# Kernel optimization log

Hardware: AMD Instinct MI355X
Metric: run time of the kernel (lower is better)

Reference implementation:

```python
import jax, jax.numpy as jnp
import numpy as np

IN_FEATURES = 4096
OUT_FEATURES = 11008
TOKENS = 4096


def setup_inputs() -> dict:
    key = jax.random.key(0)
    k1, k2, k3, k4 = jax.random.split(key, 4)
    x = jax.random.normal(k1, (TOKENS, IN_FEATURES), dtype=jnp.float32)
    # two int4 nibbles per byte; aligned_in == IN_FEATURES (already multiple of 64)
    weight_packed = jax.random.randint(k2, (OUT_FEATURES, IN_FEATURES // 2), 0, 256, dtype=jnp.int32).astype(jnp.uint8)
    scale = jax.random.uniform(k3, (OUT_FEATURES, 1), dtype=jnp.float32, minval=0.005, maxval=0.02)
    zero = jax.random.uniform(k4, (OUT_FEATURES, 1), dtype=jnp.float32, minval=0.0, maxval=15.0)
    return {"x": x, "weight_packed": weight_packed, "scale": scale, "zero": zero}


def reference(x, weight_packed, scale, zero):
    # unpack nibbles, low_first order (default OMNICODER_INT4_NIBBLE_ORDER)
    low = (weight_packed & jnp.uint8(0x0F)).astype(jnp.float32)
    high = ((weight_packed >> 4) & jnp.uint8(0x0F)).astype(jnp.float32)
    # (O, K/2, 2) -> (O, K): interleave [low, high] per byte
    nibbles = jnp.stack((low, high), axis=-1).reshape(weight_packed.shape[0], -1)
    # dequantize with per-output-channel scale/zero
    w = (nibbles - zero) * scale          # (O, aligned_in)
    w = w[:, :IN_FEATURES]                # trim alignment padding (no-op here)
    return x @ w.T                        # (TOKENS, O)
```

## Files before the change

### kernel.cpp

```cpp
#include <hip/hip_runtime.h>
#include <hip/hip_fp16.h>
#include <stdint.h>

#define TOKENS 4096
#define IN_F   4096
#define OUT_F  11008

typedef _Float16 half8 __attribute__((ext_vector_type(8)));
typedef float    f32x4 __attribute__((ext_vector_type(4)));

union H4 { __half2 h2[2]; uint2 u2; };
union H8 { __half2 h2[4]; uint4 u4; };

#define GLOAD16(g, l) __builtin_amdgcn_global_load_lds(                      \
    (const __attribute__((address_space(1))) uint32_t*)(g),                  \
    (__attribute__((address_space(3))) uint32_t*)(l), 16, 0, 0)

__global__ __launch_bounds__(256)
void convert_x_kernel(const float* __restrict__ x, __half* __restrict__ x16)
{
  const size_t i = ((size_t)blockIdx.x * 256 + threadIdx.x) * 8;
  const float4 a = *reinterpret_cast<const float4*>(x + i);
  const float4 b = *reinterpret_cast<const float4*>(x + i + 4);
  H8 r;
  r.h2[0] = __floats2half2_rn(a.x, a.y);
  r.h2[1] = __floats2half2_rn(a.z, a.w);
  r.h2[2] = __floats2half2_rn(b.x, b.y);
  r.h2[3] = __floats2half2_rn(b.z, b.w);
  *reinterpret_cast<uint4*>(x16 + i) = r.u4;
}

__global__ __launch_bounds__(256)
void dequant_w_kernel(const int* __restrict__ wq,
                      const float* __restrict__ scale,
                      const float* __restrict__ zero,
                      __half* __restrict__ w16)
{
  const size_t i = ((size_t)blockIdx.x * 256 + threadIdx.x) * 4;
  const int row = (int)(i >> 11);
  const float s  = scale[row];
  const float nb = -zero[row] * s;
  const int4 v = *reinterpret_cast<const int4*>(wq + i);
  H8 r;
  r.h2[0] = __floats2half2_rn(fmaf((float)(v.x & 15), s, nb),
                              fmaf((float)((v.x >> 4) & 15), s, nb));
  r.h2[1] = __floats2half2_rn(fmaf((float)(v.y & 15), s, nb),
                              fmaf((float)((v.y >> 4) & 15), s, nb));
  r.h2[2] = __floats2half2_rn(fmaf((float)(v.z & 15), s, nb),
                              fmaf((float)((v.z >> 4) & 15), s, nb));
  r.h2[3] = __floats2half2_rn(fmaf((float)(v.w & 15), s, nb),
                              fmaf((float)((v.w >> 4) & 15), s, nb));
  *reinterpret_cast<uint4*>(w16 + i * 2) = r.u4;
}


#define VMW4 asm volatile("s_waitcnt vmcnt(4)" ::: "memory")

#define STAGE_A(H, K0, LB)                                                    \
  do {                                                                        \
    GLOAD16(apst + (H) * 128 * IN_F + (K0), &smem[(LB) + c0 * 512]);          \
    GLOAD16(apst + (H) * 128 * IN_F + 8 * IN_F + (K0),                        \
            &smem[(LB) + c0 * 512 + 512]);                                    \
  } while (0)

#define STAGE_B(H, K0, LB)                                                    \
  do {                                                                        \
    GLOAD16(bpst + (H) * 128 * IN_F + (K0), &smem[(LB) + c0 * 512]);          \
    GLOAD16(bpst + (H) * 128 * IN_F + 8 * IN_F + (K0),                        \
            &smem[(LB) + c0 * 512 + 512]);                                    \
  } while (0)

#define PHASE(BUF, MB, READB, STAGE_STMT, DOWAIT)                             \
  do {                                                                        \
    const int _ar = arootA + (BUF) * 32768;                                   \
    const int _br = brootB + (BUF) * 32768;                                   \
    if (READB) {                                                              \
      _Pragma("unroll")                                                       \
      for (int _j = 0; _j < 4; ++_j) {                                        \
        const int _rh = bn_rh + _j * 16;                                      \
        bfr[_j][0] = *(const half8*)&smem[_br + _rh * 64 + acol0];            \
        bfr[_j][1] = *(const half8*)&smem[_br + _rh * 64 + acol1];            \
      }                                                                       \
    }                                                                         \
    half8 _af[2][2];                                                          \
    _Pragma("unroll")                                                         \
    for (int _ii = 0; _ii < 2; ++_ii) {                                       \
      const int _rh = am_rh + ((MB) * 2 + _ii) * 16;                          \
      _af[_ii][0] = *(const half8*)&smem[_ar + _rh * 64 + acol0];             \
      _af[_ii][1] = *(const half8*)&smem[_ar + _rh * 64 + acol1];             \
    }                                                                         \
    STAGE_STMT;                                                               \
    __builtin_amdgcn_sched_barrier(0);                                        \
    __builtin_amdgcn_s_barrier();                                             \
    asm volatile("s_waitcnt lgkmcnt(0)" ::: "memory");                        \
    __builtin_amdgcn_sched_barrier(0);                                        \
    __builtin_amdgcn_s_setprio(1);                                            \
    _Pragma("unroll")                                                         \
    for (int _ii = 0; _ii < 2; ++_ii)                                         \
      _Pragma("unroll")                                                       \
      for (int _j = 0; _j < 4; ++_j) {                                        \
        acc[(MB) * 2 + _ii][_j] = __builtin_amdgcn_mfma_f32_16x16x32_f16(     \
            _af[_ii][0], bfr[_j][0], acc[(MB) * 2 + _ii][_j], 0, 0, 0);       \
        acc[(MB) * 2 + _ii][_j] = __builtin_amdgcn_mfma_f32_16x16x32_f16(     \
            _af[_ii][1], bfr[_j][1], acc[(MB) * 2 + _ii][_j], 0, 0, 0);       \
      }                                                                       \
    __builtin_amdgcn_s_setprio(0);                                            \
    if (DOWAIT) { VMW4; }                                                     \
    __builtin_amdgcn_sched_barrier(0);                                        \
    __builtin_amdgcn_s_barrier();                                             \
  } while (0)

__global__ __launch_bounds__(512, 2)
void gemm256_kernel(const __half* __restrict__ A16,
                    const __half* __restrict__ W16,
                    float* __restrict__ out)
{
  __shared__ __half smem[65536];

  const int bid = blockIdx.x;
  const int wg  = (bid & 7) * 86 + (bid >> 3);
  const int mt  = wg / 43;
  const int nt  = wg - mt * 43;
  const int m0  = mt * 256;
  const int n0  = nt * 256;

  const int tid  = threadIdx.x;
  const int lane = tid & 63;
  const int wave = tid >> 6;
  const int wr   = wave >> 2;
  const int wc   = wave & 3;
  const int fm   = lane & 15;
  const int q4   = lane >> 4;

  const int swz   = (fm & 7) << 3;
  const int acol0 = (q4 * 8) ^ swz;
  const int acol1 = (32 + q4 * 8) ^ swz;
  const int arootA = wr * 8192;
  const int brootB = 16384 + (wc >> 1) * 8192;
  const int am_rh  = fm;
  const int bn_rh  = (wc & 1) * 64 + fm;

  const int c0 = wave * 2;
  const int sr = lane >> 3;
  const int sc = ((lane & 7) ^ sr) * 8;
  const __half* apst = A16 + (size_t)(m0 + c0 * 8 + sr) * IN_F + sc;
  const __half* bpst = W16 + (size_t)(n0 + c0 * 8 + sr) * IN_F + sc;

  f32x4 acc[8][4];
#pragma unroll
  for (int i = 0; i < 8; ++i)
#pragma unroll
    for (int j = 0; j < 4; ++j)
      acc[i][j] = (f32x4){0.f, 0.f, 0.f, 0.f};

  half8 bfr[4][2];

  STAGE_B(0, 0, 16384);
  STAGE_B(1, 0, 16384 + 8192);
  STAGE_A(0, 0, 0);
  STAGE_A(1, 0, 8192);
  STAGE_B(0, 64, 32768 + 16384);
  STAGE_B(1, 64, 32768 + 16384 + 8192);
  VMW4;
  __builtin_amdgcn_sched_barrier(0);
  __builtin_amdgcn_s_barrier();

#pragma unroll 1
  for (int it = 0; it < 32; ++it) {
    const int k_o = (it * 2 + 1) * 64;
    const int ke2 = ((it * 2 + 2) & 63) * 64;
    const int ko2 = ((it * 2 + 3) & 63) * 64;
    PHASE(0, 0, 1, STAGE_A(0, k_o, 32768 + 0),            0);
    PHASE(0, 1, 0, STAGE_A(1, k_o, 32768 + 8192),         0);
    PHASE(0, 2, 0, STAGE_B(0, ke2, 16384),                0);
    PHASE(0, 3, 0, STAGE_B(1, ke2, 16384 + 8192),         1);
    PHASE(1, 0, 1, STAGE_A(0, ke2, 0),                    0);
    PHASE(1, 1, 0, STAGE_A(1, ke2, 8192),                 0);
    PHASE(1, 2, 0, STAGE_B(0, ko2, 32768 + 16384),        0);
    PHASE(1, 3, 0, STAGE_B(1, ko2, 32768 + 16384 + 8192), 1);
  }

  asm volatile("s_waitcnt vmcnt(0)" ::: "memory");

  const int mbase = m0 + wr * 128 + q4 * 4;
  const int nbase = n0 + wc * 64 + fm;
#pragma unroll
  for (int i = 0; i < 8; ++i) {
#pragma unroll
    for (int j = 0; j < 4; ++j) {
#pragma unroll
      for (int r = 0; r < 4; ++r) {
        out[(size_t)(mbase + i * 16 + r) * OUT_F + (nbase + j * 16)] = acc[i][j][r];
      }
    }
  }
}

#define BM  128
#define BN  128
#define BK  32
#define LDT 40
#define NKT (IN_F / BK)

__device__ inline __half2 dequant_byte(int v, __half2 s2, __half2 b2) {
  float lo = (float)(v & 15);
  float hi = (float)((v >> 4) & 15);
  return __hfma2(__floats2half2_rn(lo, hi), s2, b2);
}

__global__ __launch_bounds__(256, 2)
void int4_gemm_kernel(const float* __restrict__ x,
                      const int* __restrict__ wq,
                      const float* __restrict__ scale,
                      const float* __restrict__ zero,
                      float* __restrict__ out)
{
  __shared__ __half As[BM * LDT];
  __shared__ __half Bs[BN * LDT];

  const int tid  = threadIdx.x;
  const int n0   = blockIdx.x * BN;
  const int m0   = blockIdx.y * BM;
  const int lane = tid & 63;
  const int wave = tid >> 6;
  const int wm   = (wave >> 1) * 64;
  const int wn   = (wave & 1) * 64;

  const int rowb  = tid >> 1;
  const int bhalf = tid & 1;
  const float s = scale[n0 + rowb];
  const float z = zero[n0 + rowb];
  const __half2 s2 = __floats2half2_rn(s, s);
  const float   nb = -z * s;
  const __half2 b2 = __floats2half2_rn(nb, nb);
  const int* wp = wq + (size_t)(n0 + rowb) * (IN_F / 2) + bhalf * 8;

  const float* xp[4];
  int arow[4], ac4[4];
#pragma unroll
  for (int i = 0; i < 4; ++i) {
    int idx = tid + i * 256;
    arow[i] = idx >> 3;
    ac4[i]  = idx & 7;
    xp[i] = x + (size_t)(m0 + arow[i]) * IN_F + ac4[i] * 4;
  }

  f32x4 acc[4][4];
#pragma unroll
  for (int i = 0; i < 4; ++i)
#pragma unroll
    for (int j = 0; j < 4; ++j)
      acc[i][j] = (f32x4){0.f, 0.f, 0.f, 0.f};

  float4 apf[4];
  int4   bpf0, bpf1;
#pragma unroll
  for (int i = 0; i < 4; ++i) apf[i] = *(const float4*)(xp[i]);
  bpf0 = *(const int4*)(wp);
  bpf1 = *(const int4*)(wp + 4);

  for (int kt = 0; kt < NKT; ++kt) {
#pragma unroll
    for (int i = 0; i < 4; ++i) {
      H4 t;
      t.h2[0] = __floats2half2_rn(apf[i].x, apf[i].y);
      t.h2[1] = __floats2half2_rn(apf[i].z, apf[i].w);
      *reinterpret_cast<uint2*>(&As[arow[i] * LDT + ac4[i] * 4]) = t.u2;
    }
    {
      H8 r0, r1;
      r0.h2[0] = dequant_byte(bpf0.x, s2, b2);
      r0.h2[1] = dequant_byte(bpf0.y, s2, b2);
      r0.h2[2] = dequant_byte(bpf0.z, s2, b2);
      r0.h2[3] = dequant_byte(bpf0.w, s2, b2);
      r1.h2[0] = dequant_byte(bpf1.x, s2, b2);
      r1.h2[1] = dequant_byte(bpf1.y, s2, b2);
      r1.h2[2] = dequant_byte(bpf1.z, s2, b2);
      r1.h2[3] = dequant_byte(bpf1.w, s2, b2);
      *reinterpret_cast<uint4*>(&Bs[rowb * LDT + bhalf * 16 + 0]) = r0.u4;
      *reinterpret_cast<uint4*>(&Bs[rowb * LDT + bhalf * 16 + 8]) = r1.u4;
    }
    if (kt + 1 < NKT) {
#pragma unroll
      for (int i = 0; i < 4; ++i) apf[i] = *(const float4*)(xp[i] + (kt + 1) * BK);
      bpf0 = *(const int4*)(wp + (size_t)(kt + 1) * 16);
      bpf1 = *(const int4*)(wp + (size_t)(kt + 1) * 16 + 4);
    }
    __syncthreads();

    const int fm = lane & 15;
    const int q4 = lane >> 4;
    half8 af[4], bf[4];
#pragma unroll
    for (int i = 0; i < 4; ++i)
      af[i] = *reinterpret_cast<const half8*>(&As[(wm + i * 16 + fm) * LDT + q4 * 8]);
#pragma unroll
    for (int j = 0; j < 4; ++j)
      bf[j] = *reinterpret_cast<const half8*>(&Bs[(wn + j * 16 + fm) * LDT + q4 * 8]);
#pragma unroll
    for (int i = 0; i < 4; ++i)
#pragma unroll
      for (int j = 0; j < 4; ++j)
        acc[i][j] = __builtin_amdgcn_mfma_f32_16x16x32_f16(af[i], bf[j], acc[i][j], 0, 0, 0);
    __syncthreads();
  }

  const int col = lane & 15;
  const int r0q = (lane >> 4) * 4;
#pragma unroll
  for (int i = 0; i < 4; ++i) {
#pragma unroll
    for (int j = 0; j < 4; ++j) {
#pragma unroll
      for (int r = 0; r < 4; ++r) {
        const int m = m0 + wm + i * 16 + r0q + r;
        const int n = n0 + wn + j * 16 + col;
        out[(size_t)m * OUT_F + n] = acc[i][j][r];
      }
    }
  }
}

extern "C" void kernel_launch(void* const* d_in, const int* in_sizes, int n_in,
                              void* d_out, int out_size, void* d_ws, size_t ws_size,
                              hipStream_t stream) {
  const float* x     = (const float*)d_in[0];
  const int*   wq    = (const int*)d_in[1];
  const float* scale = (const float*)d_in[2];
  const float* zero  = (const float*)d_in[3];
  float* out = (float*)d_out;

  const size_t X16_BYTES = (size_t)TOKENS * IN_F * sizeof(__half);
  const size_t W16_BYTES = (size_t)OUT_F * IN_F * sizeof(__half);

  if (ws_size >= X16_BYTES + W16_BYTES) {
    __half* x16 = (__half*)d_ws;
    __half* w16 = (__half*)((char*)d_ws + X16_BYTES);
    convert_x_kernel<<<(TOKENS * IN_F / 8) / 256, 256, 0, stream>>>(x, x16);
    dequant_w_kernel<<<(OUT_F * (IN_F / 2) / 4) / 256, 256, 0, stream>>>(wq, scale, zero, w16);
    gemm256_kernel<<<dim3((OUT_F / 256) * (TOKENS / 256)), 512, 0, stream>>>(x16, w16, out);
  } else {
    dim3 grid(OUT_F / BN, TOKENS / BM);
    int4_gemm_kernel<<<grid, 256, 0, stream>>>(x, wq, scale, zero, out);
  }
}
```

Baseline: 619.4 us.

## Interleave A rows across waves for per-phase waits and merge prepass kernels

The GEMM now assigns A rows to waves in an interleaved way, so the first two phases of each buffer read only the first 128-row half of A and the last two read only the second half. This lets every phase use a uniform `s_waitcnt vmcnt(6)` instead of one `vmcnt(4)` every fourth phase. The goal is finer-grained overlap between asynchronous global-to-LDS loads and MFMA work, and the output indexing is updated to match the new mapping. Separately, the x conversion and weight dequant kernels are merged into one launch to save launch overhead. The cost is a wait and barrier in every phase, which may add stalls if loads are not yet ready.

```diff
diff --git a/kernel.cpp b/kernel.cpp
--- a/kernel.cpp
+++ b/kernel.cpp
@@ -16,45 +16,49 @@
     (const __attribute__((address_space(1))) uint32_t*)(g),                  \
     (__attribute__((address_space(3))) uint32_t*)(l), 16, 0, 0)
 
+#define XCONV_BLOCKS  (TOKENS * IN_F / 8 / 256)
+#define WDEQ_BLOCKS   (OUT_F * (IN_F / 2) / 4 / 256)
+
 __global__ __launch_bounds__(256)
-void convert_x_kernel(const float* __restrict__ x, __half* __restrict__ x16)
+void prepass_kernel(const float* __restrict__ x,
+                    const int* __restrict__ wq,
+                    const float* __restrict__ scale,
+                    const float* __restrict__ zero,
+                    __half* __restrict__ x16,
+                    __half* __restrict__ w16)
 {
-  const size_t i = ((size_t)blockIdx.x * 256 + threadIdx.x) * 8;
-  const float4 a = *reinterpret_cast<const float4*>(x + i);
-  const float4 b = *reinterpret_cast<const float4*>(x + i + 4);
-  H8 r;
-  r.h2[0] = __floats2half2_rn(a.x, a.y);
-  r.h2[1] = __floats2half2_rn(a.z, a.w);
-  r.h2[2] = __floats2half2_rn(b.x, b.y);
-  r.h2[3] = __floats2half2_rn(b.z, b.w);
-  *reinterpret_cast<uint4*>(x16 + i) = r.u4;
-}
-
-__global__ __launch_bounds__(256)
-void dequant_w_kernel(const int* __restrict__ wq,
-                      const float* __restrict__ scale,
-                      const float* __restrict__ zero,
-                      __half* __restrict__ w16)
-{
-  const size_t i = ((size_t)blockIdx.x * 256 + threadIdx.x) * 4;
-  const int row = (int)(i >> 11);
-  const float s  = scale[row];
-  const float nb = -zero[row] * s;
-  const int4 v = *reinterpret_cast<const int4*>(wq + i);
-  H8 r;
-  r.h2[0] = __floats2half2_rn(fmaf((float)(v.x & 15), s, nb),
-                              fmaf((float)((v.x >> 4) & 15), s, nb));
-  r.h2[1] = __floats2half2_rn(fmaf((float)(v.y & 15), s, nb),
-                              fmaf((float)((v.y >> 4) & 15), s, nb));
-  r.h2[2] = __floats2half2_rn(fmaf((float)(v.z & 15), s, nb),
-                              fmaf((float)((v.z >> 4) & 15), s, nb));
-  r.h2[3] = __floats2half2_rn(fmaf((float)(v.w & 15), s, nb),
-                              fmaf((float)((v.w >> 4) & 15), s, nb));
-  *reinterpret_cast<uint4*>(w16 + i * 2) = r.u4;
-}
-
-
-#define VMW4 asm volatile("s_waitcnt vmcnt(4)" ::: "memory")
+  const int b = blockIdx.x;
+  if (b < XCONV_BLOCKS) {
+    const size_t i = ((size_t)b * 256 + threadIdx.x) * 8;
+    const float4 a = *reinterpret_cast<const float4*>(x + i);
+    const float4 c = *reinterpret_cast<const float4*>(x + i + 4);
+    H8 r;
+    r.h2[0] = __floats2half2_rn(a.x, a.y);
+    r.h2[1] = __floats2half2_rn(a.z, a.w);
+    r.h2[2] = __floats2half2_rn(c.x, c.y);
+    r.h2[3] = __floats2half2_rn(c.z, c.w);
+    *reinterpret_cast<uint4*>(x16 + i) = r.u4;
+  } else {
+    const size_t i = ((size_t)(b - XCONV_BLOCKS) * 256 + threadIdx.x) * 4;
+    const int row = (int)(i >> 11);
+    const float s  = scale[row];
+    const float nb = -zero[row] * s;
+    const int4 v = *reinterpret_cast<const int4*>(wq + i);
+    H8 r;
+    r.h2[0] = __floats2half2_rn(fmaf((float)(v.x & 15), s, nb),
+                                fmaf((float)((v.x >> 4) & 15), s, nb));
+    r.h2[1] = __floats2half2_rn(fmaf((float)(v.y & 15), s, nb),
+                                fmaf((float)((v.y >> 4) & 15), s, nb));
+    r.h2[2] = __floats2half2_rn(fmaf((float)(v.z & 15), s, nb),
+                                fmaf((float)((v.z >> 4) & 15), s, nb));
+    r.h2[3] = __floats2half2_rn(fmaf((float)(v.w & 15), s, nb),
+                                fmaf((float)((v.w >> 4) & 15), s, nb));
+    *reinterpret_cast<uint4*>(w16 + i * 2) = r.u4;
+  }
+}
+
+
+#define VMW6 asm volatile("s_waitcnt vmcnt(6)" ::: "memory")
 
 #define STAGE_A(H, K0, LB)                                                    \
   do {                                                                        \
@@ -70,9 +74,9 @@
             &smem[(LB) + c0 * 512 + 512]);                                    \
   } while (0)
 
-#define PHASE(BUF, MB, READB, STAGE_STMT, DOWAIT)                             \
+#define PHASE(BUF, MB, READB, STAGE_STMT)                                     \
   do {                                                                        \
-    const int _ar = arootA + (BUF) * 32768;                                   \
+    const int _ar = (BUF) * 32768;                                            \
     const int _br = brootB + (BUF) * 32768;                                   \
     if (READB) {                                                              \
       _Pragma("unroll")                                                       \
@@ -85,7 +89,7 @@
     half8 _af[2][2];                                                          \
     _Pragma("unroll")                                                         \
     for (int _ii = 0; _ii < 2; ++_ii) {                                       \
-      const int _rh = am_rh + ((MB) * 2 + _ii) * 16;                          \
+      const int _rh = am_rh + (MB) * 64 + _ii * 32;                           \
       _af[_ii][0] = *(const half8*)&smem[_ar + _rh * 64 + acol0];             \
       _af[_ii][1] = *(const half8*)&smem[_ar + _rh * 64 + acol1];             \
     }                                                                         \
@@ -105,7 +109,7 @@
             _af[_ii][1], bfr[_j][1], acc[(MB) * 2 + _ii][_j], 0, 0, 0);       \
       }                                                                       \
     __builtin_amdgcn_s_setprio(0);                                            \
-    if (DOWAIT) { VMW4; }                                                     \
+    VMW6;                                                                     \
     __builtin_amdgcn_sched_barrier(0);                                        \
     __builtin_amdgcn_s_barrier();                                             \
   } while (0)
@@ -135,9 +139,8 @@
   const int swz   = (fm & 7) << 3;
   const int acol0 = (q4 * 8) ^ swz;
   const int acol1 = (32 + q4 * 8) ^ swz;
-  const int arootA = wr * 8192;
   const int brootB = 16384 + (wc >> 1) * 8192;
-  const int am_rh  = fm;
+  const int am_rh  = wr * 16 + fm;
   const int bn_rh  = (wc & 1) * 64 + fm;
 
   const int c0 = wave * 2;
@@ -161,7 +164,7 @@
   STAGE_A(1, 0, 8192);
   STAGE_B(0, 64, 32768 + 16384);
   STAGE_B(1, 64, 32768 + 16384 + 8192);
-  VMW4;
+  asm volatile("s_waitcnt vmcnt(4)" ::: "memory");
   __builtin_amdgcn_sched_barrier(0);
   __builtin_amdgcn_s_barrier();
 
@@ -170,19 +173,19 @@
     const int k_o = (it * 2 + 1) * 64;
     const int ke2 = ((it * 2 + 2) & 63) * 64;
     const int ko2 = ((it * 2 + 3) & 63) * 64;
-    PHASE(0, 0, 1, STAGE_A(0, k_o, 32768 + 0),            0);
-    PHASE(0, 1, 0, STAGE_A(1, k_o, 32768 + 8192),         0);
-    PHASE(0, 2, 0, STAGE_B(0, ke2, 16384),                0);
-    PHASE(0, 3, 0, STAGE_B(1, ke2, 16384 + 8192),         1);
-    PHASE(1, 0, 1, STAGE_A(0, ke2, 0),                    0);
-    PHASE(1, 1, 0, STAGE_A(1, ke2, 8192),                 0);
-    PHASE(1, 2, 0, STAGE_B(0, ko2, 32768 + 16384),        0);
-    PHASE(1, 3, 0, STAGE_B(1, ko2, 32768 + 16384 + 8192), 1);
+    PHASE(0, 0, 1, STAGE_A(0, k_o, 32768 + 0));
+    PHASE(0, 1, 0, STAGE_A(1, k_o, 32768 + 8192));
+    PHASE(0, 2, 0, STAGE_B(0, ke2, 16384));
+    PHASE(0, 3, 0, STAGE_B(1, ke2, 16384 + 8192));
+    PHASE(1, 0, 1, STAGE_A(0, ke2, 0));
+    PHASE(1, 1, 0, STAGE_A(1, ke2, 8192));
+    PHASE(1, 2, 0, STAGE_B(0, ko2, 32768 + 16384));
+    PHASE(1, 3, 0, STAGE_B(1, ko2, 32768 + 16384 + 8192));
   }
 
   asm volatile("s_waitcnt vmcnt(0)" ::: "memory");
 
-  const int mbase = m0 + wr * 128 + q4 * 4;
+  const int mbase = m0 + wr * 16 + q4 * 4;
   const int nbase = n0 + wc * 64 + fm;
 #pragma unroll
   for (int i = 0; i < 8; ++i) {
@@ -190,7 +193,7 @@
     for (int j = 0; j < 4; ++j) {
 #pragma unroll
       for (int r = 0; r < 4; ++r) {
-        out[(size_t)(mbase + i * 16 + r) * OUT_F + (nbase + j * 16)] = acc[i][j][r];
+        out[(size_t)(mbase + i * 32 + r) * OUT_F + (nbase + j * 16)] = acc[i][j][r];
       }
     }
   }
@@ -336,8 +339,7 @@
   if (ws_size >= X16_BYTES + W16_BYTES) {
     __half* x16 = (__half*)d_ws;
     __half* w16 = (__half*)((char*)d_ws + X16_BYTES);
-    convert_x_kernel<<<(TOKENS * IN_F / 8) / 256, 256, 0, stream>>>(x, x16);
-    dequant_w_kernel<<<(OUT_F * (IN_F / 2) / 4) / 256, 256, 0, stream>>>(wq, scale, zero, w16);
+    prepass_kernel<<<XCONV_BLOCKS + WDEQ_BLOCKS, 256, 0, stream>>>(x, wq, scale, zero, x16, w16);
     gemm256_kernel<<<dim3((OUT_F / 256) * (TOKENS / 256)), 512, 0, stream>>>(x16, w16, out);
   } else {
     dim3 grid(OUT_F / BN, TOKENS / BM);
```

After: 607.9 us. About the same (-1.9%).
